# Performance work log

Measured on AMD Instinct MI355X. Metric: run time of the kernel, lower is better.

Reference implementation:

```python
import jax, jax.numpy as jnp
import numpy as np

ALPHA = 1.0

def setup_inputs() -> dict:
    key = jax.random.key(0)
    kx, kd = jax.random.split(key)
    B, L, D = 64, 256, 512
    x = jax.random.normal(kx, (B, L, D), dtype=jnp.float32)
    duration = jax.random.randint(kd, (B, L), 0, 8, dtype=jnp.int32)
    max_length = 1792  # L * max_duration
    return {"x": x, "duration": duration, "max_length": max_length}

def reference(x, duration, max_length):
    B, L, D = x.shape
    # round(duration * alpha) -> integer durations
    d = jnp.round(duration.astype(jnp.float32) * ALPHA).astype(jnp.int32)
    # rows with all-zero durations get one frame (original picks a random
    # position; we deterministically use position 0)
    row_sum = d.sum(axis=1)  # [B]
    d = jnp.where((row_sum == 0)[:, None] & (jnp.arange(L) == 0)[None, :], 1, d)
    # cumulative end offsets per phoneme: cum[b, j] = sum_{k<=j} d[b, k]
    cum = jnp.cumsum(d, axis=1)  # [B, L]
    t = jnp.arange(max_length)   # [T]
    # output frame t belongs to phoneme j where cum[j-1] <= t < cum[j]
    idx = jax.vmap(lambda c: jnp.searchsorted(c, t, side='right'))(cum)  # [B, T]
    idx = jnp.clip(idx, 0, L - 1)
    out = jnp.take_along_axis(x, idx[:, :, None], axis=1)  # [B, T, D]
    # zero-pad beyond each sequence's total length
    mask = (t[None, :] < cum[:, -1:]).astype(x.dtype)  # [B, T]
    out = out * mask[:, :, None]
    return out, max_length
```

## Files before the change

kernel.cpp:

```cpp
#include <hip/hip_runtime.h>


#define BB 64
#define LL 256
#define DD 512
#define TT 1792
#define D4 (DD / 4)
#define TILE 32

typedef float vfloat4 __attribute__((ext_vector_type(4)));

__global__ __launch_bounds__(256) void length_regulator_kernel(
    const vfloat4* __restrict__ x4,
    const int*     __restrict__ dur,
    const int*     __restrict__ maxlen,
    float*         __restrict__ out)
{
    __shared__ int cum[LL];
    __shared__ int sidx[TILE];
    const int tid = threadIdx.x;
    const int b   = blockIdx.y;
    const int t0  = blockIdx.x * TILE;

    cum[tid] = dur[b * LL + tid];
    __syncthreads();
    #pragma unroll
    for (int off = 1; off < LL; off <<= 1) {
        int v = (tid >= off) ? cum[tid - off] : 0;
        __syncthreads();
        cum[tid] += v;
        __syncthreads();
    }
    int total = cum[LL - 1];
    if (total == 0) cum[tid] = 1;
    __syncthreads();
    total = cum[LL - 1];

    if (tid < TILE) sidx[tid] = 0;
    __syncthreads();
    {
        const int end   = cum[tid];
        const int start = (tid == 0) ? 0 : cum[tid - 1];
        const int s = max(start, t0);
        const int e = min(end, t0 + TILE);
        for (int t = s; t < e; ++t) sidx[t - t0] = tid;
    }
    __syncthreads();

    vfloat4* out4 = (vfloat4*)out;
    const int group = tid >> 7;
    const int lane  = tid & 127;

    #pragma unroll
    for (int j = 0; j < TILE / 2; ++j) {
        const int t = t0 + j * 2 + group;
        vfloat4 val = (vfloat4)(0.f);
        if (t < total) {
            val = x4[((size_t)b * LL + sidx[t - t0]) * D4 + lane];
        }
        __builtin_nontemporal_store(val, &out4[((size_t)b * TT + t) * D4 + lane]);
    }

    if (b == 0 && blockIdx.x == 0 && tid == 0) {
        out[(size_t)BB * TT * DD] = (float)maxlen[0];
    }
}

extern "C" void kernel_launch(void* const* d_in, const int* in_sizes, int n_in,
                              void* d_out, int out_size, void* d_ws, size_t ws_size,
                              hipStream_t stream) {
    const vfloat4* x4  = (const vfloat4*)d_in[0];
    const int*     dur = (const int*)d_in[1];
    const int*     ml  = (const int*)d_in[2];
    float*         out = (float*)d_out;

    dim3 grid(TT / TILE, BB);
    length_regulator_kernel<<<grid, dim3(256), 0, stream>>>(x4, dur, ml, out);
}
```

Before: 271.6 us.

## Precompute per-row totals in a separate kernel and skip scans for padding tiles

A small first kernel reduces the durations of each row to a total length (forcing it to 1 for all-zero rows) and writes the max_length scalar. The expand kernel reads that total and, for tiles lying entirely past the sequence end, writes zeros straight away without the shared-memory prefix scan. The tile size doubles to 64 frames per block, which halves the number of blocks and repeated scans, and the copy loop is only partially unrolled. The cost is an extra kernel launch with its dependency and less block-level parallelism, in a kernel dominated by output stores.

```diff
diff --git a/kernel.cpp b/kernel.cpp
--- a/kernel.cpp
+++ b/kernel.cpp
@@ -6,24 +6,62 @@
 #define DD 512
 #define TT 1792
 #define D4 (DD / 4)
-#define TILE 32
+#define TILE 64
 
 typedef float vfloat4 __attribute__((ext_vector_type(4)));
 
-__global__ __launch_bounds__(256) void length_regulator_kernel(
+__global__ __launch_bounds__(256) void row_totals_kernel(
+    const int* __restrict__ dur,
+    const int* __restrict__ maxlen,
+    int*       __restrict__ totals,
+    float*     __restrict__ out)
+{
+    __shared__ int red[256];
+    const int b = blockIdx.x, tid = threadIdx.x;
+    red[tid] = dur[b * LL + tid];
+    __syncthreads();
+    #pragma unroll
+    for (int off = 128; off > 0; off >>= 1) {
+        if (tid < off) red[tid] += red[tid + off];
+        __syncthreads();
+    }
+    if (tid == 0) {
+        const int s = red[0];
+        totals[b] = (s == 0) ? 1 : s;
+        if (b == 0) out[(size_t)BB * TT * DD] = (float)maxlen[0];
+    }
+}
+
+__global__ __launch_bounds__(256) void expand_kernel(
     const vfloat4* __restrict__ x4,
     const int*     __restrict__ dur,
-    const int*     __restrict__ maxlen,
+    const int*     __restrict__ totals,
     float*         __restrict__ out)
 {
+    const int tid   = threadIdx.x;
+    const int b     = blockIdx.y;
+    const int t0    = blockIdx.x * TILE;
+    const int total = totals[b];
+    vfloat4* out4   = (vfloat4*)out;
+    const int group = tid >> 7;
+    const int lane  = tid & 127;
+
+    if (t0 >= total) {
+        const vfloat4 z = (vfloat4)(0.f);
+        #pragma unroll
+        for (int j = 0; j < TILE / 2; ++j) {
+            const int t = t0 + j * 2 + group;
+            __builtin_nontemporal_store(z, &out4[((size_t)b * TT + t) * D4 + lane]);
+        }
+        return;
+    }
+
     __shared__ int cum[LL];
     __shared__ int sidx[TILE];
-    const int tid = threadIdx.x;
-    const int b   = blockIdx.y;
-    const int t0  = blockIdx.x * TILE;
+    cum[tid] = dur[b * LL + tid];
+    if (tid < TILE) sidx[tid] = 0;
+    __syncthreads();
 
-    cum[tid] = dur[b * LL + tid];
-    __syncthreads();
     #pragma unroll
     for (int off = 1; off < LL; off <<= 1) {
         int v = (tid >= off) ? cum[tid - off] : 0;
@@ -31,13 +69,9 @@
         cum[tid] += v;
         __syncthreads();
     }
-    int total = cum[LL - 1];
-    if (total == 0) cum[tid] = 1;
+    if (cum[LL - 1] == 0) cum[tid] = 1;
     __syncthreads();
-    total = cum[LL - 1];
 
-    if (tid < TILE) sidx[tid] = 0;
-    __syncthreads();
     {
         const int end   = cum[tid];
         const int start = (tid == 0) ? 0 : cum[tid - 1];
@@ -47,22 +81,14 @@
     }
     __syncthreads();
 
-    vfloat4* out4 = (vfloat4*)out;
-    const int group = tid >> 7;
-    const int lane  = tid & 127;
-
-    #pragma unroll
+    #pragma unroll 8
     for (int j = 0; j < TILE / 2; ++j) {
         const int t = t0 + j * 2 + group;
         vfloat4 val = (vfloat4)(0.f);
         if (t < total) {
-            val = x4[((size_t)b * LL + sidx[t - t0]) * D4 + lane];
+            val = x4[((size_t)b * LL + sidx[j * 2 + group]) * D4 + lane];
         }
         __builtin_nontemporal_store(val, &out4[((size_t)b * TT + t) * D4 + lane]);
-    }
-
-    if (b == 0 && blockIdx.x == 0 && tid == 0) {
-        out[(size_t)BB * TT * DD] = (float)maxlen[0];
     }
 }
 
@@ -73,7 +99,8 @@
     const int*     dur = (const int*)d_in[1];
     const int*     ml  = (const int*)d_in[2];
     float*         out = (float*)d_out;
+    int*           tot = (int*)d_ws;
 
-    dim3 grid(TT / TILE, BB);
-    length_regulator_kernel<<<grid, dim3(256), 0, stream>>>(x4, dur, ml, out);
+    row_totals_kernel<<<dim3(BB), dim3(256), 0, stream>>>(dur, ml, tot, out);
+    expand_kernel<<<dim3(TT / TILE, BB), dim3(256), 0, stream>>>(x4, dur, tot, out);
 }
```

Result: no change. 275.9 us (+1.6%).
